# Kernel optimization log

Hardware: AMD Instinct MI355X
Metric: run time of the kernel (lower is better)

The kernel has to match this reference:

```python
import jax, jax.numpy as jnp
import numpy as np

D_MODEL, D_STATE, D_CONV, D_INNER, DT_RANK = 96, 16, 3, 192, 6
BATCH, H, W = 4, 64, 64


def setup_inputs() -> dict:
    key = jax.random.key(0)
    ks = jax.random.split(key, 8)
    s = 0.02
    return {
        "x": jax.random.normal(ks[0], (BATCH, H, W, D_MODEL), jnp.float32),
        "in_proj_w": jax.random.normal(ks[1], (2 * D_INNER, D_MODEL), jnp.float32) * s,
        "conv_w": jax.random.normal(ks[2], (D_INNER, 1, D_CONV, D_CONV), jnp.float32) * s,
        "conv_b": jnp.zeros((D_INNER,), jnp.float32),
        "x_proj_w": jax.random.normal(ks[3], (4, DT_RANK + 2 * D_STATE, D_INNER), jnp.float32) * s,
        "dt_w": jax.random.normal(ks[4], (4, D_INNER, DT_RANK), jnp.float32) * s,
        # dt bias ~ inverse-softplus of dt in [1e-3, 1e-1] (roughly log-uniform negative values)
        "dt_b": jax.random.uniform(ks[5], (4, D_INNER), jnp.float32, minval=-6.0, maxval=-2.3),
        "A_logs": jnp.log(jnp.tile(jnp.arange(1, D_STATE + 1, dtype=jnp.float32), (4 * D_INNER, 1))),
        "Ds": jnp.ones((4 * D_INNER,), jnp.float32),
        "ln_w": jnp.ones((D_INNER,), jnp.float32),
        "ln_b": jnp.zeros((D_INNER,), jnp.float32),
        "out_proj_w": jax.random.normal(ks[6], (D_MODEL, D_INNER), jnp.float32) * s,
    }


def _ss2d(x, in_proj_w, conv_w, conv_b, x_proj_w, dt_w, dt_b, A_logs, Ds, ln_w, ln_b, out_proj_w):
    B, Hh, Ww, C = x.shape
    D = conv_w.shape[0]          # d_inner
    N = A_logs.shape[1]          # d_state
    R = dt_w.shape[2]            # dt_rank
    L = Hh * Ww
    K = 4

    xz = x @ in_proj_w.T                          # (B,H,W,2D)
    xi, z = jnp.split(xz, 2, axis=-1)
    xc = jnp.transpose(xi, (0, 3, 1, 2))          # (B,D,H,W)
    pad = (D_CONV - 1) // 2
    xc = jax.lax.conv_general_dilated(xc, conv_w, (1, 1), ((pad, pad), (pad, pad)),
                                      feature_group_count=D)
    xc = jax.nn.silu(xc + conv_b[None, :, None, None])

    # 4 scan directions: row-major, col-major, and their reverses
    x_flat = xc.reshape(B, D, L)
    x_tr = jnp.transpose(xc, (0, 1, 3, 2)).reshape(B, D, L)
    x_hwwh = jnp.stack([x_flat, x_tr], axis=1)                     # (B,2,D,L)
    xs = jnp.concatenate([x_hwwh, jnp.flip(x_hwwh, axis=-1)], axis=1)  # (B,K,D,L)

    x_dbl = jnp.einsum('bkdl,kcd->bkcl', xs, x_proj_w)
    dts, Bs, Cs = jnp.split(x_dbl, [R, R + N], axis=2)             # (B,K,R,L),(B,K,N,L),(B,K,N,L)
    dts = jnp.einsum('bkrl,kdr->bkdl', dts, dt_w)
    delta = jax.nn.softplus(dts + dt_b[None, :, :, None])          # (B,K,D,L)
    A = -jnp.exp(A_logs).reshape(K, D, N)                          # (K,D,N)

    # sequential selective scan over L (L-first for lax.scan)
    u_seq = jnp.moveaxis(xs, -1, 0)        # (L,B,K,D)
    dt_seq = jnp.moveaxis(delta, -1, 0)    # (L,B,K,D)
    B_seq = jnp.moveaxis(Bs, -1, 0)        # (L,B,K,N)
    C_seq = jnp.moveaxis(Cs, -1, 0)        # (L,B,K,N)

    def step(h, inp):
        u_t, dt_t, B_t, C_t = inp
        h = jnp.exp(dt_t[..., None] * A) * h + (dt_t * u_t)[..., None] * B_t[:, :, None, :]
        y = jnp.einsum('bkdn,bkn->bkd', h, C_t)
        return h, y

    h0 = jnp.zeros((B, K, D, N), jnp.float32)
    _, ys = jax.lax.scan(step, h0, (u_seq, dt_seq, B_seq, C_seq))
    out_y = jnp.moveaxis(ys, 0, -1) + Ds.reshape(K, D)[None, :, :, None] * xs  # (B,K,D,L)

    y1 = out_y[:, 0]
    y2 = jnp.transpose(out_y[:, 1].reshape(B, D, Ww, Hh), (0, 1, 3, 2)).reshape(B, D, L)
    y3 = jnp.flip(out_y[:, 2], axis=-1)
    y4 = jnp.transpose(jnp.flip(out_y[:, 3], axis=-1).reshape(B, D, Ww, Hh), (0, 1, 3, 2)).reshape(B, D, L)
    y = y1 + y2 + y3 + y4                                           # (B,D,L)

    y = jnp.transpose(y, (0, 2, 1)).reshape(B, Hh, Ww, D)
    mu = y.mean(-1, keepdims=True)
    var = y.var(-1, keepdims=True)
    y = (y - mu) * jax.lax.rsqrt(var + 1e-5) * ln_w + ln_b
    y = y * jax.nn.silu(z)
    return y @ out_proj_w.T


def reference(x, in_proj_w, conv_w, conv_b, x_proj_w, dt_w, dt_b, A_logs, Ds, ln_w, ln_b, out_proj_w):
    return _ss2d(x, in_proj_w, conv_w, conv_b, x_proj_w, dt_w, dt_b, A_logs, Ds, ln_w, ln_b, out_proj_w)
```

## Files before the change

kernel.cpp:

```cpp
#include <hip/hip_runtime.h>

constexpr int BATCH = 4;
constexpr int HS    = 64;
constexpr int WSZ   = 64;
constexpr int LSEQ  = 4096;
constexpr int DM    = 96;
constexpr int DI    = 192;
constexpr int NS    = 16;
constexpr int RK    = 6;
constexpr int KD    = 4;
constexpr int NCH   = 128;
constexpr int CLEN  = 32;
constexpr int XDS   = 160;
constexpr int GCH   = 16;
constexpr int GLEN  = NCH / GCH;

__device__ __forceinline__ int pos_of(int k, int l) {
  switch (k & 3) {
    case 0: return l;
    case 1: return ((l & 63) << 6) | (l >> 6);
    case 2: return LSEQ - 1 - l;
    default: { int lp = LSEQ - 1 - l; return ((lp & 63) << 6) | (lp >> 6); }
  }
}

__device__ __forceinline__ float softplus_f(float s) {
  return (s > 20.f) ? s : __logf(1.f + __expf(s));
}

__device__ __forceinline__ void pw16(float e, float* p) {
  float e2 = e * e, e4 = e2 * e2, e8 = e4 * e4;
  p[1] = e;       p[2] = e2;      p[3] = e2 * e;  p[4] = e4;
  p[5] = e4 * e;  p[6] = e4 * e2; p[7] = p[6] * e; p[8] = e8;
  p[9] = e8 * e;  p[10] = e8 * e2; p[11] = p[10] * e; p[12] = e8 * e4;
  p[13] = p[12] * e; p[14] = p[12] * e2; p[15] = p[14] * e; p[16] = e8 * e8;
}

__device__ __forceinline__ bool geo_check(const float* Al) {
  const float lntab[16] = {0.f, 0.6931472f, 1.0986123f, 1.3862944f, 1.6094379f,
                           1.7917595f, 1.9459101f, 2.0794415f, 2.1972246f, 2.3025851f,
                           2.3978953f, 2.4849066f, 2.5649494f, 2.6390573f, 2.7080502f,
                           2.7725887f};
  bool g = true;
  #pragma unroll
  for (int n = 0; n < NS; ++n)
    g = g && (fabsf(Al[n] - Al[0] - lntab[n]) <= 2e-3f);
  return g;
}

__device__ __forceinline__ float dt6(const float* w, float bsv, float4 t0, float4 t1) {
  return bsv + w[0]*t0.x + w[1]*t0.y + w[2]*t0.z + w[3]*t0.w + w[4]*t1.x + w[5]*t1.y;
}

__launch_bounds__(256)
__global__ void transpose_w(const float* __restrict__ in, float* __restrict__ outp,
                            int R, int C_) {
  int idx = blockIdx.x * 256 + threadIdx.x;
  if (idx < R * C_) {
    int r = idx / C_, c = idx % C_;
    outp[(size_t)c * R + r] = in[idx];
  }
}

template <int NN, int KK, int TM, int KT>
__launch_bounds__(256)
__global__ void gemm_nt(const float* __restrict__ A, const float* __restrict__ BT,
                        float* __restrict__ C, int M) {
  constexpr int TN  = 64;
  constexpr int RPT = TM / 16;
  constexpr int SA  = KT + 4;
  constexpr int KQ  = KT / 4;
  __shared__ float As[TM][SA];
  __shared__ float Bs[KT][TN];
  const int t = threadIdx.x;
  const int row0 = blockIdx.y * TM;
  const int col0 = blockIdx.x * TN;
  const int tc = t & 15;
  const int tr = t >> 4;

  float acc[RPT][4];
  #pragma unroll
  for (int i = 0; i < RPT; ++i)
    { acc[i][0]=0.f; acc[i][1]=0.f; acc[i][2]=0.f; acc[i][3]=0.f; }

  for (int k0 = 0; k0 < KK; k0 += KT) {
    #pragma unroll 1
    for (int idx = t; idx < TM * KQ; idx += 256) {
      int r = idx / KQ, kq = idx % KQ;
      *(float4*)&As[r][kq * 4] =
          *(const float4*)&A[(size_t)(row0 + r) * KK + k0 + kq * 4];
    }
    #pragma unroll 1
    for (int idx = t; idx < KT * 16; idx += 256) {
      int kk = idx >> 4, cq = idx & 15;
      int col = col0 + cq * 4;
      float4 v = make_float4(0.f, 0.f, 0.f, 0.f);
      if (col < NN) v = *(const float4*)&BT[(size_t)(k0 + kk) * NN + col];
      *(float4*)&Bs[kk][cq * 4] = v;
    }
    __syncthreads();
    #pragma unroll 4
    for (int kk = 0; kk < KT; ++kk) {
      float4 bv = *(const float4*)&Bs[kk][tc * 4];
      #pragma unroll
      for (int i = 0; i < RPT; ++i) {
        float a = As[tr * RPT + i][kk];
        acc[i][0] += a * bv.x; acc[i][1] += a * bv.y;
        acc[i][2] += a * bv.z; acc[i][3] += a * bv.w;
      }
    }
    __syncthreads();
  }
  int c = col0 + tc * 4;
  if (c < NN) {
    #pragma unroll
    for (int i = 0; i < RPT; ++i) {
      size_t r0 = (size_t)(row0 + tr * RPT + i) * NN + c;
      *(float4*)&C[r0] = make_float4(acc[i][0], acc[i][1], acc[i][2], acc[i][3]);
    }
  }
}

__launch_bounds__(256)
__global__ void conv_silu(const float* __restrict__ xz, const float* __restrict__ cw,
                          const float* __restrict__ cb, float* __restrict__ xc) {
  int idx = blockIdx.x * 256 + threadIdx.x;
  int d = idx % DI;
  int p = (idx / DI) % LSEQ;
  int b = idx / (DI * LSEQ);
  int h = p >> 6, w = p & 63;
  float acc = cb[d];
  #pragma unroll
  for (int kh = 0; kh < 3; ++kh) {
    int hh = h + kh - 1;
    if ((unsigned)hh >= (unsigned)HS) continue;
    #pragma unroll
    for (int kw = 0; kw < 3; ++kw) {
      int ww = w + kw - 1;
      if ((unsigned)ww >= (unsigned)WSZ) continue;
      acc += xz[((size_t)b * LSEQ + (hh << 6) + ww) * (2 * DI) + d] * cw[d * 9 + kh * 3 + kw];
    }
  }
  xc[idx] = acc / (1.f + __expf(-acc));
}

__launch_bounds__(256)
__global__ void build_wcatT(const float* __restrict__ xw, float* __restrict__ WcatT) {
  int idx = blockIdx.x * 256 + threadIdx.x;
  int col = idx / XDS, j = idx % XDS;
  int k = j / 40, jj = j % 40;
  float v = 0.f;
  int src = -1;
  if (jj < 16)      src = k * 38 + 6 + jj;
  else if (jj < 32) src = k * 38 + 22 + (jj - 16);
  else if (jj < 38) src = k * 38 + (jj - 32);
  if (src >= 0) v = xw[(size_t)src * DI + col];
  WcatT[idx] = v;
}

__launch_bounds__(192)
__global__ void scan_phase1(const float* __restrict__ xc, const float* __restrict__ xdbl,
                            const float* __restrict__ Alog, const float* __restrict__ dtw,
                            const float* __restrict__ dtb,
                            float* __restrict__ hN, float* __restrict__ sumdB) {
  const int d = threadIdx.x;
  const int ch = blockIdx.x, k = blockIdx.y, b = blockIdx.z;
  const int bk = b * KD + k;
  __shared__ float4 Bsh[CLEN * 6];
  {
    int idx = d;
    int j = idx / 6, q = idx % 6;
    int p = pos_of(k, ch * CLEN + j);
    int qq = (q < 4) ? q : (q + 4);
    Bsh[idx] = *(const float4*)&xdbl[(size_t)(b * LSEQ + p) * XDS + k * 40 + qq * 4];
  }
  float Al[NS];
  {
    const float4* Ap = (const float4*)&Alog[((size_t)k * DI + d) * NS];
    #pragma unroll
    for (int q = 0; q < 4; ++q) {
      float4 a = Ap[q];
      Al[q*4+0] = a.x; Al[q*4+1] = a.y; Al[q*4+2] = a.z; Al[q*4+3] = a.w;
    }
  }
  const bool geo = geo_check(Al);
  const float An0 = -__expf(Al[0]);
  float w[RK];
  #pragma unroll
  for (int r = 0; r < RK; ++r) w[r] = dtw[((size_t)k * DI + d) * RK + r];
  const float bsv = dtb[k * DI + d];
  __syncthreads();

  float h[NS];
  #pragma unroll
  for (int n = 0; n < NS; ++n) h[n] = 0.f;
  float sumd = 0.f;
  const int l0 = ch * CLEN;
  if (geo) {
    #pragma unroll 2
    for (int j = 0; j < CLEN; ++j) {
      const int p = pos_of(k, l0 + j);
      const size_t bp = (size_t)b * LSEQ + p;
      float4 t0 = Bsh[j * 6 + 4], t1 = Bsh[j * 6 + 5];
      float dl = softplus_f(dt6(w, bsv, t0, t1));
      float du = dl * xc[bp * DI + d];
      float pw[17];
      pw16(__expf(dl * An0), pw);
      #pragma unroll
      for (int q = 0; q < 4; ++q) {
        float4 v = Bsh[j * 6 + q];
        h[q*4+0] = pw[q*4+1] * h[q*4+0] + du * v.x;
        h[q*4+1] = pw[q*4+2] * h[q*4+1] + du * v.y;
        h[q*4+2] = pw[q*4+3] * h[q*4+2] + du * v.z;
        h[q*4+3] = pw[q*4+4] * h[q*4+3] + du * v.w;
      }
      sumd += dl;
    }
  } else {
    float An[NS];
    #pragma unroll
    for (int n = 0; n < NS; ++n) An[n] = -__expf(Al[n]);
    #pragma unroll 1
    for (int j = 0; j < CLEN; ++j) {
      const int p = pos_of(k, l0 + j);
      const size_t bp = (size_t)b * LSEQ + p;
      float4 t0 = Bsh[j * 6 + 4], t1 = Bsh[j * 6 + 5];
      float dl = softplus_f(dt6(w, bsv, t0, t1));
      float du = dl * xc[bp * DI + d];
      #pragma unroll
      for (int q = 0; q < 4; ++q) {
        float4 v = Bsh[j * 6 + q];
        h[q*4+0] = __expf(dl * An[q*4+0]) * h[q*4+0] + du * v.x;
        h[q*4+1] = __expf(dl * An[q*4+1]) * h[q*4+1] + du * v.y;
        h[q*4+2] = __expf(dl * An[q*4+2]) * h[q*4+2] + du * v.z;
        h[q*4+3] = __expf(dl * An[q*4+3]) * h[q*4+3] + du * v.w;
      }
      sumd += dl;
    }
  }
  const size_t o = ((size_t)bk * NCH + ch) * DI + d;
  float4* Hp = (float4*)&hN[o * NS];
  #pragma unroll
  for (int q = 0; q < 4; ++q)
    Hp[q] = make_float4(h[q*4+0], h[q*4+1], h[q*4+2], h[q*4+3]);
  sumdB[o] = sumd;
}

__launch_bounds__(256)
__global__ void combine_a(const float* __restrict__ hN, const float* __restrict__ sumdB,
                          const float* __restrict__ Alog,
                          float* __restrict__ Wg, float* __restrict__ Tg) {
  const int tid = blockIdx.x * 256 + threadIdx.x;
  const int n  = tid & 15;
  int rem = tid >> 4;
  const int d  = rem % DI;  rem /= DI;
  const int g  = rem % GCH;
  const int bk = rem / GCH;
  const int k  = bk & 3;
  const float An = -__expf(Alog[((size_t)k * DI + d) * NS + n]);
  float W = 1.f, T = 0.f;
  #pragma unroll
  for (int j = 0; j < GLEN; ++j) {
    const int c = g * GLEN + j;
    const size_t o = ((size_t)bk * NCH + c) * DI + d;
    float w = __expf(An * sumdB[o]);
    T = hN[o * NS + n] + w * T;
    W *= w;
  }
  Wg[tid] = W;
  Tg[tid] = T;
}

__launch_bounds__(256)
__global__ void combine_b(const float* __restrict__ Wg, const float* __restrict__ Tg,
                          float* __restrict__ Hg) {
  const int tid = blockIdx.x * 256 + threadIdx.x;
  const int dn = tid & (DI * NS - 1);
  const int bk = tid / (DI * NS);
  float H = 0.f;
  #pragma unroll
  for (int g = 0; g < GCH; ++g) {
    const size_t o = ((size_t)(bk * GCH + g)) * (DI * NS) + dn;
    Hg[o] = H;
    H = Tg[o] + Wg[o] * H;
  }
}

__launch_bounds__(256)
__global__ void combine_c(float* __restrict__ hN, const float* __restrict__ sumdB,
                          const float* __restrict__ Alog, const float* __restrict__ Hg) {
  const int tid = blockIdx.x * 256 + threadIdx.x;
  const int n  = tid & 15;
  int rem = tid >> 4;
  const int d  = rem % DI;  rem /= DI;
  const int g  = rem % GCH;
  const int bk = rem / GCH;
  const int k  = bk & 3;
  const float An = -__expf(Alog[((size_t)k * DI + d) * NS + n]);
  float e = Hg[tid];
  #pragma unroll
  for (int j = 0; j < GLEN; ++j) {
    const int c = g * GLEN + j;
    const size_t o = ((size_t)bk * NCH + c) * DI + d;
    float w = __expf(An * sumdB[o]);
    float tmp = hN[o * NS + n];
    hN[o * NS + n] = e;
    e = tmp + w * e;
  }
}

__launch_bounds__(192)
__global__ void scan_phase2(const float* __restrict__ xc, const float* __restrict__ xdbl,
                            const float* __restrict__ Alog, const float* __restrict__ dtw,
                            const float* __restrict__ dtb, const float* __restrict__ hin,
                            float* __restrict__ ypl) {
  const int d = threadIdx.x;
  const int ch = blockIdx.x, k = blockIdx.y, b = blockIdx.z;
  const int bk = b * KD + k;
  __shared__ float4 Bsh[CLEN * 10];
  #pragma unroll 1
  for (int idx = d; idx < CLEN * 10; idx += 192) {
    int j = idx / 10, q = idx % 10;
    int p = pos_of(k, ch * CLEN + j);
    Bsh[idx] = *(const float4*)&xdbl[(size_t)(b * LSEQ + p) * XDS + k * 40 + q * 4];
  }
  float Al[NS];
  {
    const float4* Ap = (const float4*)&Alog[((size_t)k * DI + d) * NS];
    #pragma unroll
    for (int q = 0; q < 4; ++q) {
      float4 a = Ap[q];
      Al[q*4+0] = a.x; Al[q*4+1] = a.y; Al[q*4+2] = a.z; Al[q*4+3] = a.w;
    }
  }
  const bool geo = geo_check(Al);
  const float An0 = -__expf(Al[0]);
  float w[RK];
  #pragma unroll
  for (int r = 0; r < RK; ++r) w[r] = dtw[((size_t)k * DI + d) * RK + r];
  const float bsv = dtb[k * DI + d];

  float h[NS];
  {
    const size_t o = ((size_t)bk * NCH + ch) * DI + d;
    const float4* Hp = (const float4*)&hin[o * NS];
    #pragma unroll
    for (int q = 0; q < 4; ++q) {
      float4 v = Hp[q];
      h[q*4+0] = v.x; h[q*4+1] = v.y; h[q*4+2] = v.z; h[q*4+3] = v.w;
    }
  }
  __syncthreads();
  float* yout = ypl + (size_t)bk * LSEQ * DI;
  const int l0 = ch * CLEN;
  if (geo) {
    #pragma unroll 2
    for (int j = 0; j < CLEN; ++j) {
      const int p = pos_of(k, l0 + j);
      const size_t bp = (size_t)b * LSEQ + p;
      float4 t0 = Bsh[j * 10 + 8], t1 = Bsh[j * 10 + 9];
      float dl = softplus_f(dt6(w, bsv, t0, t1));
      float du = dl * xc[bp * DI + d];
      float pw[17];
      pw16(__expf(dl * An0), pw);
      float y = 0.f;
      #pragma unroll
      for (int q = 0; q < 4; ++q) {
        float4 v  = Bsh[j * 10 + q];
        float4 c4 = Bsh[j * 10 + 4 + q];
        h[q*4+0] = pw[q*4+1] * h[q*4+0] + du * v.x; y += h[q*4+0] * c4.x;
        h[q*4+1] = pw[q*4+2] * h[q*4+1] + du * v.y; y += h[q*4+1] * c4.y;
        h[q*4+2] = pw[q*4+3] * h[q*4+2] + du * v.z; y += h[q*4+2] * c4.z;
        h[q*4+3] = pw[q*4+4] * h[q*4+3] + du * v.w; y += h[q*4+3] * c4.w;
      }
      yout[(size_t)p * DI + d] = y;
    }
  } else {
    float An[NS];
    #pragma unroll
    for (int n = 0; n < NS; ++n) An[n] = -__expf(Al[n]);
    #pragma unroll 1
    for (int j = 0; j < CLEN; ++j) {
      const int p = pos_of(k, l0 + j);
      const size_t bp = (size_t)b * LSEQ + p;
      float4 t0 = Bsh[j * 10 + 8], t1 = Bsh[j * 10 + 9];
      float dl = softplus_f(dt6(w, bsv, t0, t1));
      float du = dl * xc[bp * DI + d];
      float y = 0.f;
      #pragma unroll
      for (int q = 0; q < 4; ++q) {
        float4 v  = Bsh[j * 10 + q];
        float4 c4 = Bsh[j * 10 + 4 + q];
        h[q*4+0] = __expf(dl * An[q*4+0]) * h[q*4+0] + du * v.x; y += h[q*4+0] * c4.x;
        h[q*4+1] = __expf(dl * An[q*4+1]) * h[q*4+1] + du * v.y; y += h[q*4+1] * c4.y;
        h[q*4+2] = __expf(dl * An[q*4+2]) * h[q*4+2] + du * v.z; y += h[q*4+2] * c4.z;
        h[q*4+3] = __expf(dl * An[q*4+3]) * h[q*4+3] + du * v.w; y += h[q*4+3] * c4.w;
      }
      yout[(size_t)p * DI + d] = y;
    }
  }
}

__launch_bounds__(192)
__global__ void fuse_ln(const float* __restrict__ ypl, const float* __restrict__ xc,
                        const float* __restrict__ Ds, const float* __restrict__ xz,
                        const float* __restrict__ lnw, const float* __restrict__ lnb,
                        float* __restrict__ ymul) {
  const int row = blockIdx.x;
  const int b = row >> 12;
  const size_t pd = (size_t)row * DI + threadIdx.x;
  const int d = threadIdx.x;
  constexpr size_t PL = (size_t)LSEQ * DI;
  float u = xc[pd];
  float sDs = Ds[d] + Ds[DI + d] + Ds[2 * DI + d] + Ds[3 * DI + d];
  const size_t base = (size_t)(b * KD) * PL + pd - (size_t)b * PL;
  float y = ypl[base] + ypl[base + PL] + ypl[base + 2 * PL] + ypl[base + 3 * PL] + sDs * u;
  float s1 = y, s2 = y * y;
  #pragma unroll
  for (int off = 32; off; off >>= 1) {
    s1 += __shfl_xor(s1, off);
    s2 += __shfl_xor(s2, off);
  }
  __shared__ float r1[3], r2[3];
  int wid = d >> 6;
  if ((d & 63) == 0) { r1[wid] = s1; r2[wid] = s2; }
  __syncthreads();
  float S1 = r1[0] + r1[1] + r1[2];
  float S2 = r2[0] + r2[1] + r2[2];
  float mu = S1 * (1.f / DI);
  float var = S2 * (1.f / DI) - mu * mu;
  float yn = (y - mu) * rsqrtf(var + 1e-5f) * lnw[d] + lnb[d];
  float zv = xz[(size_t)row * (2 * DI) + DI + d];
  float g = zv / (1.f + __expf(-zv));
  ymul[pd] = yn * g;
}

extern "C" void kernel_launch(void* const* d_in, const int* in_sizes, int n_in,
                              void* d_out, int out_size, void* d_ws, size_t ws_size,
                              hipStream_t stream) {
  (void)in_sizes; (void)n_in; (void)out_size; (void)ws_size;
  const float* x          = (const float*)d_in[0];
  const float* in_proj_w  = (const float*)d_in[1];
  const float* conv_w     = (const float*)d_in[2];
  const float* conv_b     = (const float*)d_in[3];
  const float* x_proj_w   = (const float*)d_in[4];
  const float* dt_w       = (const float*)d_in[5];
  const float* dt_b       = (const float*)d_in[6];
  const float* A_logs     = (const float*)d_in[7];
  const float* Ds         = (const float*)d_in[8];
  const float* ln_w       = (const float*)d_in[9];
  const float* ln_b       = (const float*)d_in[10];
  const float* out_proj_w = (const float*)d_in[11];
  float* out = (float*)d_out;
  float* ws  = (float*)d_ws;

  constexpr size_t SZ_XZ    = (size_t)BATCH * LSEQ * 2 * DI;
  constexpr size_t SZ_XC    = (size_t)BATCH * LSEQ * DI;
  constexpr size_t SZ_XD    = (size_t)BATCH * LSEQ * XDS;
  constexpr size_t SZ_HN    = (size_t)BATCH * KD * NCH * DI * NS;
  constexpr size_t SZ_SUMD  = (size_t)BATCH * KD * NCH * DI;
  constexpr size_t SZ_YPL   = (size_t)BATCH * KD * LSEQ * DI;
  constexpr size_t SZ_G     = (size_t)BATCH * KD * GCH * DI * NS;

  float* xz    = ws;
  float* xc    = xz + SZ_XZ;
  float* xdbl  = xc + SZ_XC;
  float* hN    = xdbl + SZ_XD;
  float* sumd  = hN + SZ_HN;
  float* ypl   = sumd + SZ_SUMD;
  float* WcatT = ypl + SZ_YPL;
  float* inpT  = WcatT + (size_t)DI * XDS;
  float* outpT = inpT + (size_t)DM * 2 * DI;
  float* Wg    = outpT + (size_t)DI * DM;
  float* Tg    = Wg + SZ_G;
  float* Hg    = Tg + SZ_G;
  float* ymul  = hN;

  const int M = BATCH * LSEQ;
  const int SG = BATCH * KD * GCH * DI * NS;

  build_wcatT<<<(DI * XDS) / 256, 256, 0, stream>>>(x_proj_w, WcatT);
  transpose_w<<<(2 * DI * DM + 255) / 256, 256, 0, stream>>>(in_proj_w, inpT, 2 * DI, DM);
  transpose_w<<<(DM * DI + 255) / 256, 256, 0, stream>>>(out_proj_w, outpT, DM, DI);
  gemm_nt<2 * DI, DM, 64, 96><<<dim3(6, M / 64), 256, 0, stream>>>(x, inpT, xz, M);
  conv_silu<<<(BATCH * LSEQ * DI) / 256, 256, 0, stream>>>(xz, conv_w, conv_b, xc);
  gemm_nt<XDS, DI, 64, 96><<<dim3(3, M / 64), 256, 0, stream>>>(xc, WcatT, xdbl, M);
  scan_phase1<<<dim3(NCH, KD, BATCH), 192, 0, stream>>>(xc, xdbl, A_logs, dt_w, dt_b,
                                                        hN, sumd);
  combine_a<<<SG / 256, 256, 0, stream>>>(hN, sumd, A_logs, Wg, Tg);
  combine_b<<<(BATCH * KD * DI * NS) / 256, 256, 0, stream>>>(Wg, Tg, Hg);
  combine_c<<<SG / 256, 256, 0, stream>>>(hN, sumd, A_logs, Hg);
  scan_phase2<<<dim3(NCH, KD, BATCH), 192, 0, stream>>>(xc, xdbl, A_logs, dt_w, dt_b,
                                                        hN, ypl);
  fuse_ln<<<M, DI, 0, stream>>>(ypl, xc, Ds, xz, ln_w, ln_b, ymul);
  gemm_nt<DM, DI, 64, 96><<<dim3(2, M / 64), 256, 0, stream>>>(ymul, outpT, out, M);
}
```

Before: 212.0 us.

## Fold local output into first scan pass and add carry-in correction pass

The first chunked scan pass now also writes each chunk's local output y (starting from zero state) alongside its end state and dt sum. The second pass is replaced by a lighter correction kernel that adds the carried-in state's contribution, using cumulative dt decay and the C vectors, via a read-modify-write of y, and it skips the first chunk. The three small weight-prep kernels are merged into one launch. The aim is to remove the full recurrence recomputation and the xc reads from the second pass, at the cost of extra ypl read-modify-write traffic and extra exp work per step in the non-geometric path.

```diff
diff --git a/kernel.cpp b/kernel.cpp
--- a/kernel.cpp
+++ b/kernel.cpp
@@ -53,12 +53,32 @@
 }
 
 __launch_bounds__(256)
-__global__ void transpose_w(const float* __restrict__ in, float* __restrict__ outp,
-                            int R, int C_) {
+__global__ void prep_weights(const float* __restrict__ xw, const float* __restrict__ ipw,
+                             const float* __restrict__ opw, float* __restrict__ WcatT,
+                             float* __restrict__ inpT, float* __restrict__ outpT) {
   int idx = blockIdx.x * 256 + threadIdx.x;
-  if (idx < R * C_) {
-    int r = idx / C_, c = idx % C_;
-    outp[(size_t)c * R + r] = in[idx];
+  if (idx < DI * XDS) {
+    int col = idx / XDS, j = idx % XDS;
+    int k = j / 40, jj = j % 40;
+    float v = 0.f;
+    int src = -1;
+    if (jj < 16)      src = k * 38 + 6 + jj;
+    else if (jj < 32) src = k * 38 + 22 + (jj - 16);
+    else if (jj < 38) src = k * 38 + (jj - 32);
+    if (src >= 0) v = xw[(size_t)src * DI + col];
+    WcatT[idx] = v;
+    return;
+  }
+  idx -= DI * XDS;
+  if (idx < 2 * DI * DM) {
+    int r = idx / DM, c = idx % DM;
+    inpT[(size_t)c * (2 * DI) + r] = ipw[idx];
+    return;
+  }
+  idx -= 2 * DI * DM;
+  if (idx < DM * DI) {
+    int r = idx / DI, c = idx % DI;
+    outpT[(size_t)c * DM + r] = opw[idx];
   }
 }
 
@@ -144,175 +164,11 @@
   xc[idx] = acc / (1.f + __expf(-acc));
 }
 
-__launch_bounds__(256)
-__global__ void build_wcatT(const float* __restrict__ xw, float* __restrict__ WcatT) {
-  int idx = blockIdx.x * 256 + threadIdx.x;
-  int col = idx / XDS, j = idx % XDS;
-  int k = j / 40, jj = j % 40;
-  float v = 0.f;
-  int src = -1;
-  if (jj < 16)      src = k * 38 + 6 + jj;
-  else if (jj < 32) src = k * 38 + 22 + (jj - 16);
-  else if (jj < 38) src = k * 38 + (jj - 32);
-  if (src >= 0) v = xw[(size_t)src * DI + col];
-  WcatT[idx] = v;
-}
-
 __launch_bounds__(192)
 __global__ void scan_phase1(const float* __restrict__ xc, const float* __restrict__ xdbl,
                             const float* __restrict__ Alog, const float* __restrict__ dtw,
                             const float* __restrict__ dtb,
-                            float* __restrict__ hN, float* __restrict__ sumdB) {
-  const int d = threadIdx.x;
-  const int ch = blockIdx.x, k = blockIdx.y, b = blockIdx.z;
-  const int bk = b * KD + k;
-  __shared__ float4 Bsh[CLEN * 6];
-  {
-    int idx = d;
-    int j = idx / 6, q = idx % 6;
-    int p = pos_of(k, ch * CLEN + j);
-    int qq = (q < 4) ? q : (q + 4);
-    Bsh[idx] = *(const float4*)&xdbl[(size_t)(b * LSEQ + p) * XDS + k * 40 + qq * 4];
-  }
-  float Al[NS];
-  {
-    const float4* Ap = (const float4*)&Alog[((size_t)k * DI + d) * NS];
-    #pragma unroll
-    for (int q = 0; q < 4; ++q) {
-      float4 a = Ap[q];
-      Al[q*4+0] = a.x; Al[q*4+1] = a.y; Al[q*4+2] = a.z; Al[q*4+3] = a.w;
-    }
-  }
-  const bool geo = geo_check(Al);
-  const float An0 = -__expf(Al[0]);
-  float w[RK];
-  #pragma unroll
-  for (int r = 0; r < RK; ++r) w[r] = dtw[((size_t)k * DI + d) * RK + r];
-  const float bsv = dtb[k * DI + d];
-  __syncthreads();
-
-  float h[NS];
-  #pragma unroll
-  for (int n = 0; n < NS; ++n) h[n] = 0.f;
-  float sumd = 0.f;
-  const int l0 = ch * CLEN;
-  if (geo) {
-    #pragma unroll 2
-    for (int j = 0; j < CLEN; ++j) {
-      const int p = pos_of(k, l0 + j);
-      const size_t bp = (size_t)b * LSEQ + p;
-      float4 t0 = Bsh[j * 6 + 4], t1 = Bsh[j * 6 + 5];
-      float dl = softplus_f(dt6(w, bsv, t0, t1));
-      float du = dl * xc[bp * DI + d];
-      float pw[17];
-      pw16(__expf(dl * An0), pw);
-      #pragma unroll
-      for (int q = 0; q < 4; ++q) {
-        float4 v = Bsh[j * 6 + q];
-        h[q*4+0] = pw[q*4+1] * h[q*4+0] + du * v.x;
-        h[q*4+1] = pw[q*4+2] * h[q*4+1] + du * v.y;
-        h[q*4+2] = pw[q*4+3] * h[q*4+2] + du * v.z;
-        h[q*4+3] = pw[q*4+4] * h[q*4+3] + du * v.w;
-      }
-      sumd += dl;
-    }
-  } else {
-    float An[NS];
-    #pragma unroll
-    for (int n = 0; n < NS; ++n) An[n] = -__expf(Al[n]);
-    #pragma unroll 1
-    for (int j = 0; j < CLEN; ++j) {
-      const int p = pos_of(k, l0 + j);
-      const size_t bp = (size_t)b * LSEQ + p;
-      float4 t0 = Bsh[j * 6 + 4], t1 = Bsh[j * 6 + 5];
-      float dl = softplus_f(dt6(w, bsv, t0, t1));
-      float du = dl * xc[bp * DI + d];
-      #pragma unroll
-      for (int q = 0; q < 4; ++q) {
-        float4 v = Bsh[j * 6 + q];
-        h[q*4+0] = __expf(dl * An[q*4+0]) * h[q*4+0] + du * v.x;
-        h[q*4+1] = __expf(dl * An[q*4+1]) * h[q*4+1] + du * v.y;
-        h[q*4+2] = __expf(dl * An[q*4+2]) * h[q*4+2] + du * v.z;
-        h[q*4+3] = __expf(dl * An[q*4+3]) * h[q*4+3] + du * v.w;
-      }
-      sumd += dl;
-    }
-  }
-  const size_t o = ((size_t)bk * NCH + ch) * DI + d;
-  float4* Hp = (float4*)&hN[o * NS];
-  #pragma unroll
-  for (int q = 0; q < 4; ++q)
-    Hp[q] = make_float4(h[q*4+0], h[q*4+1], h[q*4+2], h[q*4+3]);
-  sumdB[o] = sumd;
-}
-
-__launch_bounds__(256)
-__global__ void combine_a(const float* __restrict__ hN, const float* __restrict__ sumdB,
-                          const float* __restrict__ Alog,
-                          float* __restrict__ Wg, float* __restrict__ Tg) {
-  const int tid = blockIdx.x * 256 + threadIdx.x;
-  const int n  = tid & 15;
-  int rem = tid >> 4;
-  const int d  = rem % DI;  rem /= DI;
-  const int g  = rem % GCH;
-  const int bk = rem / GCH;
-  const int k  = bk & 3;
-  const float An = -__expf(Alog[((size_t)k * DI + d) * NS + n]);
-  float W = 1.f, T = 0.f;
-  #pragma unroll
-  for (int j = 0; j < GLEN; ++j) {
-    const int c = g * GLEN + j;
-    const size_t o = ((size_t)bk * NCH + c) * DI + d;
-    float w = __expf(An * sumdB[o]);
-    T = hN[o * NS + n] + w * T;
-    W *= w;
-  }
-  Wg[tid] = W;
-  Tg[tid] = T;
-}
-
-__launch_bounds__(256)
-__global__ void combine_b(const float* __restrict__ Wg, const float* __restrict__ Tg,
-                          float* __restrict__ Hg) {
-  const int tid = blockIdx.x * 256 + threadIdx.x;
-  const int dn = tid & (DI * NS - 1);
-  const int bk = tid / (DI * NS);
-  float H = 0.f;
-  #pragma unroll
-  for (int g = 0; g < GCH; ++g) {
-    const size_t o = ((size_t)(bk * GCH + g)) * (DI * NS) + dn;
-    Hg[o] = H;
-    H = Tg[o] + Wg[o] * H;
-  }
-}
-
-__launch_bounds__(256)
-__global__ void combine_c(float* __restrict__ hN, const float* __restrict__ sumdB,
-                          const float* __restrict__ Alog, const float* __restrict__ Hg) {
-  const int tid = blockIdx.x * 256 + threadIdx.x;
-  const int n  = tid & 15;
-  int rem = tid >> 4;
-  const int d  = rem % DI;  rem /= DI;
-  const int g  = rem % GCH;
-  const int bk = rem / GCH;
-  const int k  = bk & 3;
-  const float An = -__expf(Alog[((size_t)k * DI + d) * NS + n]);
-  float e = Hg[tid];
-  #pragma unroll
-  for (int j = 0; j < GLEN; ++j) {
-    const int c = g * GLEN + j;
-    const size_t o = ((size_t)bk * NCH + c) * DI + d;
-    float w = __expf(An * sumdB[o]);
-    float tmp = hN[o * NS + n];
-    hN[o * NS + n] = e;
-    e = tmp + w * e;
-  }
-}
-
-__launch_bounds__(192)
-__global__ void scan_phase2(const float* __restrict__ xc, const float* __restrict__ xdbl,
-                            const float* __restrict__ Alog, const float* __restrict__ dtw,
-                            const float* __restrict__ dtb, const float* __restrict__ hin,
+                            float* __restrict__ hN, float* __restrict__ sumdB,
                             float* __restrict__ ypl) {
   const int d = threadIdx.x;
   const int ch = blockIdx.x, k = blockIdx.y, b = blockIdx.z;
@@ -339,18 +195,12 @@
   #pragma unroll
   for (int r = 0; r < RK; ++r) w[r] = dtw[((size_t)k * DI + d) * RK + r];
   const float bsv = dtb[k * DI + d];
+  __syncthreads();
 
   float h[NS];
-  {
-    const size_t o = ((size_t)bk * NCH + ch) * DI + d;
-    const float4* Hp = (const float4*)&hin[o * NS];
-    #pragma unroll
-    for (int q = 0; q < 4; ++q) {
-      float4 v = Hp[q];
-      h[q*4+0] = v.x; h[q*4+1] = v.y; h[q*4+2] = v.z; h[q*4+3] = v.w;
-    }
-  }
-  __syncthreads();
+  #pragma unroll
+  for (int n = 0; n < NS; ++n) h[n] = 0.f;
+  float sumd = 0.f;
   float* yout = ypl + (size_t)bk * LSEQ * DI;
   const int l0 = ch * CLEN;
   if (geo) {
@@ -373,6 +223,7 @@
         h[q*4+2] = pw[q*4+3] * h[q*4+2] + du * v.z; y += h[q*4+2] * c4.z;
         h[q*4+3] = pw[q*4+4] * h[q*4+3] + du * v.w; y += h[q*4+3] * c4.w;
       }
+      sumd += dl;
       yout[(size_t)p * DI + d] = y;
     }
   } else {
@@ -396,7 +247,164 @@
         h[q*4+2] = __expf(dl * An[q*4+2]) * h[q*4+2] + du * v.z; y += h[q*4+2] * c4.z;
         h[q*4+3] = __expf(dl * An[q*4+3]) * h[q*4+3] + du * v.w; y += h[q*4+3] * c4.w;
       }
+      sumd += dl;
       yout[(size_t)p * DI + d] = y;
+    }
+  }
+  const size_t o = ((size_t)bk * NCH + ch) * DI + d;
+  float4* Hp = (float4*)&hN[o * NS];
+  #pragma unroll
+  for (int q = 0; q < 4; ++q)
+    Hp[q] = make_float4(h[q*4+0], h[q*4+1], h[q*4+2], h[q*4+3]);
+  sumdB[o] = sumd;
+}
+
+__launch_bounds__(256)
+__global__ void combine_a(const float* __restrict__ hN, const float* __restrict__ sumdB,
+                          const float* __restrict__ Alog,
+                          float* __restrict__ Wg, float* __restrict__ Tg) {
+  const int tid = blockIdx.x * 256 + threadIdx.x;
+  const int n  = tid & 15;
+  int rem = tid >> 4;
+  const int d  = rem % DI;  rem /= DI;
+  const int g  = rem % GCH;
+  const int bk = rem / GCH;
+  const int k  = bk & 3;
+  const float An = -__expf(Alog[((size_t)k * DI + d) * NS + n]);
+  float W = 1.f, T = 0.f;
+  #pragma unroll
+  for (int j = 0; j < GLEN; ++j) {
+    const int c = g * GLEN + j;
+    const size_t o = ((size_t)bk * NCH + c) * DI + d;
+    float w = __expf(An * sumdB[o]);
+    T = hN[o * NS + n] + w * T;
+    W *= w;
+  }
+  Wg[tid] = W;
+  Tg[tid] = T;
+}
+
+__launch_bounds__(256)
+__global__ void combine_b(const float* __restrict__ Wg, const float* __restrict__ Tg,
+                          float* __restrict__ Hg) {
+  const int tid = blockIdx.x * 256 + threadIdx.x;
+  const int dn = tid & (DI * NS - 1);
+  const int bk = tid / (DI * NS);
+  float H = 0.f;
+  #pragma unroll
+  for (int g = 0; g < GCH; ++g) {
+    const size_t o = ((size_t)(bk * GCH + g)) * (DI * NS) + dn;
+    Hg[o] = H;
+    H = Tg[o] + Wg[o] * H;
+  }
+}
+
+__launch_bounds__(256)
+__global__ void combine_c(float* __restrict__ hN, const float* __restrict__ sumdB,
+                          const float* __restrict__ Alog, const float* __restrict__ Hg) {
+  const int tid = blockIdx.x * 256 + threadIdx.x;
+  const int n  = tid & 15;
+  int rem = tid >> 4;
+  const int d  = rem % DI;  rem /= DI;
+  const int g  = rem % GCH;
+  const int bk = rem / GCH;
+  const int k  = bk & 3;
+  const float An = -__expf(Alog[((size_t)k * DI + d) * NS + n]);
+  float e = Hg[tid];
+  #pragma unroll
+  for (int j = 0; j < GLEN; ++j) {
+    const int c = g * GLEN + j;
+    const size_t o = ((size_t)bk * NCH + c) * DI + d;
+    float w = __expf(An * sumdB[o]);
+    float tmp = hN[o * NS + n];
+    hN[o * NS + n] = e;
+    e = tmp + w * e;
+  }
+}
+
+__launch_bounds__(192)
+__global__ void scan_corr(const float* __restrict__ xdbl, const float* __restrict__ Alog,
+                          const float* __restrict__ dtw, const float* __restrict__ dtb,
+                          const float* __restrict__ hin, float* __restrict__ ypl) {
+  const int d = threadIdx.x;
+  const int ch = blockIdx.x + 1;
+  const int k = blockIdx.y, b = blockIdx.z;
+  const int bk = b * KD + k;
+  __shared__ float4 Bsh[CLEN * 6];
+  {
+    int idx = d;
+    int j = idx / 6, q = idx % 6;
+    int p = pos_of(k, ch * CLEN + j);
+    Bsh[idx] = *(const float4*)&xdbl[(size_t)(b * LSEQ + p) * XDS + k * 40 + (q + 4) * 4];
+  }
+  float Al[NS];
+  {
+    const float4* Ap = (const float4*)&Alog[((size_t)k * DI + d) * NS];
+    #pragma unroll
+    for (int q = 0; q < 4; ++q) {
+      float4 a = Ap[q];
+      Al[q*4+0] = a.x; Al[q*4+1] = a.y; Al[q*4+2] = a.z; Al[q*4+3] = a.w;
+    }
+  }
+  const bool geo = geo_check(Al);
+  const float An0 = -__expf(Al[0]);
+  float w[RK];
+  #pragma unroll
+  for (int r = 0; r < RK; ++r) w[r] = dtw[((size_t)k * DI + d) * RK + r];
+  const float bsv = dtb[k * DI + d];
+
+  float g[NS];
+  {
+    const size_t o = ((size_t)bk * NCH + ch) * DI + d;
+    const float4* Hp = (const float4*)&hin[o * NS];
+    #pragma unroll
+    for (int q = 0; q < 4; ++q) {
+      float4 v = Hp[q];
+      g[q*4+0] = v.x; g[q*4+1] = v.y; g[q*4+2] = v.z; g[q*4+3] = v.w;
+    }
+  }
+  __syncthreads();
+  float* yout = ypl + (size_t)bk * LSEQ * DI;
+  const int l0 = ch * CLEN;
+  float cum = 0.f;
+  if (geo) {
+    #pragma unroll 2
+    for (int j = 0; j < CLEN; ++j) {
+      const int p = pos_of(k, l0 + j);
+      float4 t0 = Bsh[j * 6 + 4], t1 = Bsh[j * 6 + 5];
+      cum += softplus_f(dt6(w, bsv, t0, t1));
+      float pw[17];
+      pw16(__expf(cum * An0), pw);
+      float y = 0.f;
+      #pragma unroll
+      for (int q = 0; q < 4; ++q) {
+        float4 c4 = Bsh[j * 6 + q];
+        y += (pw[q*4+1] * g[q*4+0]) * c4.x;
+        y += (pw[q*4+2] * g[q*4+1]) * c4.y;
+        y += (pw[q*4+3] * g[q*4+2]) * c4.z;
+        y += (pw[q*4+4] * g[q*4+3]) * c4.w;
+      }
+      yout[(size_t)p * DI + d] += y;
+    }
+  } else {
+    float An[NS];
+    #pragma unroll
+    for (int n = 0; n < NS; ++n) An[n] = -__expf(Al[n]);
+    #pragma unroll 1
+    for (int j = 0; j < CLEN; ++j) {
+      const int p = pos_of(k, l0 + j);
+      float4 t0 = Bsh[j * 6 + 4], t1 = Bsh[j * 6 + 5];
+      cum += softplus_f(dt6(w, bsv, t0, t1));
+      float y = 0.f;
+      #pragma unroll
+      for (int q = 0; q < 4; ++q) {
+        float4 c4 = Bsh[j * 6 + q];
+        y += (__expf(An[q*4+0] * cum) * g[q*4+0]) * c4.x;
+        y += (__expf(An[q*4+1] * cum) * g[q*4+1]) * c4.y;
+        y += (__expf(An[q*4+2] * cum) * g[q*4+2]) * c4.z;
+        y += (__expf(An[q*4+3] * cum) * g[q*4+3]) * c4.w;
+      }
+      yout[(size_t)p * DI + d] += y;
     }
   }
 }
@@ -478,20 +486,20 @@
 
   const int M = BATCH * LSEQ;
   const int SG = BATCH * KD * GCH * DI * NS;
-
-  build_wcatT<<<(DI * XDS) / 256, 256, 0, stream>>>(x_proj_w, WcatT);
-  transpose_w<<<(2 * DI * DM + 255) / 256, 256, 0, stream>>>(in_proj_w, inpT, 2 * DI, DM);
-  transpose_w<<<(DM * DI + 255) / 256, 256, 0, stream>>>(out_proj_w, outpT, DM, DI);
+  const int PREP = DI * XDS + 2 * DI * DM + DM * DI;
+
+  prep_weights<<<(PREP + 255) / 256, 256, 0, stream>>>(x_proj_w, in_proj_w, out_proj_w,
+                                                       WcatT, inpT, outpT);
   gemm_nt<2 * DI, DM, 64, 96><<<dim3(6, M / 64), 256, 0, stream>>>(x, inpT, xz, M);
   conv_silu<<<(BATCH * LSEQ * DI) / 256, 256, 0, stream>>>(xz, conv_w, conv_b, xc);
   gemm_nt<XDS, DI, 64, 96><<<dim3(3, M / 64), 256, 0, stream>>>(xc, WcatT, xdbl, M);
   scan_phase1<<<dim3(NCH, KD, BATCH), 192, 0, stream>>>(xc, xdbl, A_logs, dt_w, dt_b,
-                                                        hN, sumd);
+                                                        hN, sumd, ypl);
   combine_a<<<SG / 256, 256, 0, stream>>>(hN, sumd, A_logs, Wg, Tg);
   combine_b<<<(BATCH * KD * DI * NS) / 256, 256, 0, stream>>>(Wg, Tg, Hg);
   combine_c<<<SG / 256, 256, 0, stream>>>(hN, sumd, A_logs, Hg);
-  scan_phase2<<<dim3(NCH, KD, BATCH), 192, 0, stream>>>(xc, xdbl, A_logs, dt_w, dt_b,
-                                                        hN, ypl);
+  scan_corr<<<dim3(NCH - 1, KD, BATCH), 192, 0, stream>>>(xdbl, A_logs, dt_w, dt_b,
+                                                          hN, ypl);
   fuse_ln<<<M, DI, 0, stream>>>(ypl, xc, Ds, xz, ln_w, ln_b, ymul);
   gemm_nt<DM, DI, 64, 96><<<dim3(2, M / 64), 256, 0, stream>>>(ymul, outpT, out, M);
 }
```

New measurement: 213.2 us. No clear change (+0.6%).
